# Performance work log

Hardware: AMD Instinct MI355X
Metric: run time of the kernel (lower is better)

The kernel has to match this reference:

```python
import jax, jax.numpy as jnp
import numpy as np

N_NODES = 50000
N_EDGES = 800000
NODE_DIM = 64
EDGE_DIM = 16
HIDDEN = 128
EPS = 1e-5


def _linear_init(key, fan_in, fan_out):
    k1, k2 = jax.random.split(key)
    bound = 1.0 / np.sqrt(fan_in)
    W = jax.random.uniform(k1, (fan_in, fan_out), minval=-bound, maxval=bound, dtype=jnp.float32)
    b = jax.random.uniform(k2, (fan_out,), minval=-bound, maxval=bound, dtype=jnp.float32)
    return W, b


def batchnorm(h, gamma, beta):
    # BatchNorm1d in training mode: batch mean/var (biased), eps=1e-5
    mu = jnp.mean(h, axis=0, keepdims=True)
    var = jnp.mean((h - mu) ** 2, axis=0, keepdims=True)
    return (h - mu) * jax.lax.rsqrt(var + EPS) * gamma + beta


def setup_inputs() -> dict:
    key = jax.random.key(0)
    ks = jax.random.split(key, 8)
    x = jax.random.normal(ks[0], (N_NODES, NODE_DIM), dtype=jnp.float32)
    edge_index = jax.random.randint(ks[1], (2, N_EDGES), 0, N_NODES, dtype=jnp.int64)
    edge_attr = jax.random.normal(ks[2], (N_EDGES, EDGE_DIM), dtype=jnp.float32)
    We1, be1 = _linear_init(ks[3], 2 * NODE_DIM + EDGE_DIM, HIDDEN)
    We2, be2 = _linear_init(ks[4], HIDDEN, HIDDEN)
    Wm, bm = _linear_init(ks[5], HIDDEN, HIDDEN)
    Wn1, bn1 = _linear_init(ks[6], NODE_DIM + HIDDEN, HIDDEN)
    Wn2, bn2 = _linear_init(ks[7], HIDDEN, HIDDEN)
    ones = jnp.ones((HIDDEN,), jnp.float32)
    zeros = jnp.zeros((HIDDEN,), jnp.float32)
    return dict(x=x, edge_index=edge_index, edge_attr=edge_attr,
                We1=We1, be1=be1, ge=ones, bbe=zeros, We2=We2, be2=be2,
                Wm=Wm, bm=bm,
                Wn1=Wn1, bn1=bn1, gn=ones, bbn=zeros, Wn2=Wn2, bn2=bn2)


def reference(x, edge_index, edge_attr, We1, be1, ge, bbe, We2, be2, Wm, bm, Wn1, bn1, gn, bbn, Wn2, bn2):
    row, col = edge_index[0], edge_index[1]
    # gather + concat -> edge network (Linear, BN, ReLU, Linear)
    edge_input = jnp.concatenate([x[row], x[col], edge_attr], axis=-1)  # [E, 2n+e]
    h = jax.nn.relu(batchnorm(edge_input @ We1 + be1, ge, bbe))
    edge_features = h @ We2 + be2
    # message MLP (Linear, ReLU)
    messages = jax.nn.relu(edge_features @ Wm + bm)  # [E, H]
    # scatter-add into source nodes
    agg = jax.ops.segment_sum(messages, row, num_segments=N_NODES)  # [N, H]
    # node network (Linear, BN, ReLU, Linear)
    node_input = jnp.concatenate([x, agg], axis=-1)
    hn = jax.nn.relu(batchnorm(node_input @ Wn1 + bn1, gn, bbn))
    return hn @ Wn2 + bn2
```

## Files before the change

kernel.cpp:

```cpp
#include <hip/hip_runtime.h>
#include <stdint.h>

#define NNODES 50000
#define NEDGES 800000
#define H 128
#define BN_EPS 1e-5f

typedef short short8 __attribute__((ext_vector_type(8)));
typedef short short4v __attribute__((ext_vector_type(4)));
typedef float f32x4 __attribute__((ext_vector_type(4)));

__device__ __forceinline__ float bf2f(unsigned short u) {
    unsigned int v = ((unsigned int)u) << 16;
    return __uint_as_float(v);
}
__device__ __forceinline__ unsigned short f2bf(float f) {
    unsigned int x = __float_as_uint(f);
    return (unsigned short)((x + 0x7FFFu + ((x >> 16) & 1u)) >> 16);
}
__device__ __forceinline__ short8 s8z() { short8 z = {0,0,0,0,0,0,0,0}; return z; }

template<int KB>
__device__ __forceinline__ void gemm_tile(const short* __restrict__ sA, const int SK,
                                          const unsigned short* __restrict__ WT, const int RK,
                                          const int n0, f32x4 acc[4][4], const int lane) {
    const int mr = lane & 15, quad = lane >> 4;
    const short* W = (const short*)WT;
    #pragma unroll
    for (int kb = 0; kb < KB; ++kb) {
        short8 a[4];
        #pragma unroll
        for (int mt = 0; mt < 4; ++mt)
            a[mt] = *(const short8*)&sA[(mt*16 + mr)*SK + kb*32 + quad*8];
        #pragma unroll
        for (int nt = 0; nt < 4; ++nt) {
            short8 b = *(const short8*)&W[(size_t)(n0 + nt*16 + mr)*RK + kb*32 + quad*8];
            #pragma unroll
            for (int mt = 0; mt < 4; ++mt)
                acc[mt][nt] = __builtin_amdgcn_mfma_f32_16x16x32_bf16(a[mt], b, acc[mt][nt], 0, 0, 0);
        }
    }
}

__global__ void k_fold(const float* __restrict__ We2, const float* __restrict__ be2,
                       const float* __restrict__ Wm, const float* __restrict__ bm,
                       float* __restrict__ W2m, float* __restrict__ b2m) {
    int j = threadIdx.x;
    int i = blockIdx.x;
    if (i < H) {
        float acc = 0.f;
        for (int k = 0; k < H; ++k) acc = fmaf(We2[i*H + k], Wm[k*H + j], acc);
        W2m[i*H + j] = acc;
    } else {
        float acc = bm[j];
        for (int k = 0; k < H; ++k) acc = fmaf(be2[k], Wm[k*H + j], acc);
        b2m[j] = acc;
    }
}

__global__ void k_prep2(const float* __restrict__ We1, const float* __restrict__ Wn1,
                        const float* __restrict__ Wn2,
                        unsigned short* __restrict__ WabT, unsigned short* __restrict__ Wn1T,
                        unsigned short* __restrict__ Wn2T, unsigned short* __restrict__ WcT,
                        int* __restrict__ cnt, float* __restrict__ S1f) {
    int i = blockIdx.x*256 + threadIdx.x;
    if (i < 16384) {
        int n = i >> 6, k = i & 63;
        WabT[n*64 + k] = f2bf(We1[(n < 128 ? k : 64 + k)*H + (n & 127)]);
    } else if (i < 40960) {
        int j = i - 16384; int n = j / 192, k = j - n*192;
        Wn1T[n*192 + k] = f2bf(Wn1[k*H + n]);
    } else if (i < 57344) {
        int j = i - 40960; int n = j >> 7, k = j & 127;
        Wn2T[n*H + k] = f2bf(Wn2[k*H + n]);
    } else if (i < 61440) {
        int j = i - 57344; int n = j >> 5, k = j & 31;
        WcT[n*32 + k] = (k < 16) ? f2bf(We1[(128 + k)*H + n]) : (unsigned short)0;
    } else if (i < 111440) {
        cnt[i - 61440] = 0;
    } else if (i < 112464) {
        S1f[i - 111440] = 0.f;
    }
}

__global__ void k_count(const int* __restrict__ ei, int* __restrict__ cnt) {
    int e = blockIdx.x*256 + threadIdx.x;
    if (e < NEDGES) atomicAdd(&cnt[ei[e]], 1);
}

__global__ void k_scanA(const int* __restrict__ cnt, int* __restrict__ bsum) {
    __shared__ int ws[4];
    const int tid = threadIdx.x;
    int i = blockIdx.x*256 + tid;
    int v = (i < NNODES) ? cnt[i] : 0;
    #pragma unroll
    for (int off = 32; off > 0; off >>= 1) v += __shfl_down(v, off);
    if ((tid & 63) == 0) ws[tid >> 6] = v;
    __syncthreads();
    if (tid == 0) bsum[blockIdx.x] = ws[0] + ws[1] + ws[2] + ws[3];
}

__global__ void k_scanB(const int* __restrict__ bsum, int* __restrict__ bpre,
                        int* __restrict__ offsets) {
    __shared__ int ws[4];
    const int tid = threadIdx.x;
    const int lane = tid & 63, wid = tid >> 6;
    int v = (tid < 196) ? bsum[tid] : 0;
    int xv = v;
    #pragma unroll
    for (int off = 1; off < 64; off <<= 1) {
        int y = __shfl_up(xv, off);
        if (lane >= off) xv += y;
    }
    if (lane == 63) ws[wid] = xv;
    __syncthreads();
    int base = 0;
    for (int w = 0; w < 4; ++w) if (w < wid) base += ws[w];
    int incl = base + xv;
    if (tid < 196) bpre[tid] = incl - v;
    if (tid == 255) offsets[NNODES] = incl;
}

__global__ void k_scanC(const int* __restrict__ cnt, const int* __restrict__ bpre,
                        int* __restrict__ offsets, int* __restrict__ cursor) {
    __shared__ int ws[4];
    const int tid = threadIdx.x;
    const int lane = tid & 63, wid = tid >> 6;
    int i = blockIdx.x*256 + tid;
    int v = (i < NNODES) ? cnt[i] : 0;
    int xv = v;
    #pragma unroll
    for (int off = 1; off < 64; off <<= 1) {
        int y = __shfl_up(xv, off);
        if (lane >= off) xv += y;
    }
    if (lane == 63) ws[wid] = xv;
    __syncthreads();
    int base = bpre[blockIdx.x];
    for (int w = 0; w < 4; ++w) if (w < wid) base += ws[w];
    int excl = base + xv - v;
    if (i < NNODES) { offsets[i] = excl; cursor[i] = excl; }
}

__global__ void k_scatter(const int* __restrict__ ei, int* __restrict__ cursor,
                          int* __restrict__ elist) {
    int e = blockIdx.x*256 + threadIdx.x;
    if (e < NEDGES) {
        int p = atomicAdd(&cursor[ei[e]], 1);
        elist[p] = e;
    }
}

__launch_bounds__(256)
__global__ void k_T(const float* __restrict__ x, const unsigned short* __restrict__ WabT,
                    unsigned short* __restrict__ T) {
    __shared__ short sA[128*72];
    const int tid = threadIdx.x;
    const int n0b = blockIdx.x*128;
    {
        const int rowl = tid >> 1, half = (tid & 1)*32;
        const int node = n0b + rowl;
        const bool ok = node < NNODES;
        #pragma unroll
        for (int c = 0; c < 4; ++c) {
            int k0 = half + c*8;
            short8 o = s8z();
            if (ok) {
                float4 a = *(const float4*)&x[node*64 + k0];
                float4 b = *(const float4*)&x[node*64 + k0 + 4];
                o[0]=(short)f2bf(a.x); o[1]=(short)f2bf(a.y); o[2]=(short)f2bf(a.z); o[3]=(short)f2bf(a.w);
                o[4]=(short)f2bf(b.x); o[5]=(short)f2bf(b.y); o[6]=(short)f2bf(b.z); o[7]=(short)f2bf(b.w);
            }
            *(short8*)&sA[rowl*72 + k0] = o;
        }
    }
    __syncthreads();
    const int wave = tid >> 6, lane = tid & 63;
    const int m0 = (wave & 1)*64;
    const int n0 = blockIdx.y*128 + (wave >> 1)*64;
    f32x4 acc[4][4];
    f32x4 z = {0.f, 0.f, 0.f, 0.f};
    #pragma unroll
    for (int mt = 0; mt < 4; ++mt)
        #pragma unroll
        for (int nt = 0; nt < 4; ++nt) acc[mt][nt] = z;
    gemm_tile<2>(sA + m0*72, 72, WabT, 64, n0, acc, lane);
    const int mr = lane & 15, quad = lane >> 4;
    #pragma unroll
    for (int nt = 0; nt < 4; ++nt) {
        int j = n0 + nt*16 + mr;
        #pragma unroll
        for (int mt = 0; mt < 4; ++mt) {
            int nb = n0b + m0 + mt*16 + quad*4;
            #pragma unroll
            for (int r = 0; r < 4; ++r) {
                int node = nb + r;
                if (node < NNODES) T[(size_t)node*256 + j] = f2bf(acc[mt][nt][r]);
            }
        }
    }
}

__launch_bounds__(256, 4)
__global__ void k_pass1(const unsigned short* __restrict__ T, const int* __restrict__ ei,
                        const int* __restrict__ elist, const float* __restrict__ ea,
                        const unsigned short* __restrict__ WcT, const float* __restrict__ be1,
                        unsigned short* __restrict__ eaP,
                        float* __restrict__ gS, float* __restrict__ gSS) {
    __shared__ short sT[128*136];
    __shared__ float sS[H], sSS[H];
    const int tid = threadIdx.x;
    const int p0 = blockIdx.x*128;
    const int wave = tid >> 6, lane = tid & 63;
    const int mr = lane & 15, quad = lane >> 4;
    const int mbase = wave*32;
    if (tid < 128) { sS[tid] = 0.f; sSS[tid] = 0.f; }
    const int lp = tid >> 1, half = tid & 1;
    const int e = elist[p0 + lp];
    const bool eaActive = (quad < 2);
    int e0i = 0, e1i = 0;
    if (eaActive) {
        e0i = elist[p0 + mbase + mr];
        e1i = elist[p0 + mbase + 16 + mr];
    }
    const int row = ei[e], col = ei[NEDGES + e];
    f32x4 u0, u1, v0, v1;
    if (eaActive) {
        u0 = __builtin_nontemporal_load((const f32x4*)&ea[(size_t)e0i*16 + quad*8]);
        u1 = __builtin_nontemporal_load((const f32x4*)&ea[(size_t)e0i*16 + quad*8 + 4]);
        v0 = __builtin_nontemporal_load((const f32x4*)&ea[(size_t)e1i*16 + quad*8]);
        v1 = __builtin_nontemporal_load((const f32x4*)&ea[(size_t)e1i*16 + quad*8 + 4]);
    }
    const unsigned short* Tr = &T[(size_t)row*256 + half*64];
    const unsigned short* Tc = &T[(size_t)col*256 + 128 + half*64];
    short8 t1[8], t2[8];
    #pragma unroll
    for (int c = 0; c < 8; ++c) t1[c] = *(const short8*)&Tr[c*8];
    #pragma unroll
    for (int c = 0; c < 8; ++c) t2[c] = *(const short8*)&Tc[c*8];
    __builtin_amdgcn_sched_barrier(0);
    short8 a0 = s8z(), a1 = s8z();
    if (eaActive) {
        a0[0]=(short)f2bf(u0[0]); a0[1]=(short)f2bf(u0[1]); a0[2]=(short)f2bf(u0[2]); a0[3]=(short)f2bf(u0[3]);
        a0[4]=(short)f2bf(u1[0]); a0[5]=(short)f2bf(u1[1]); a0[6]=(short)f2bf(u1[2]); a0[7]=(short)f2bf(u1[3]);
        a1[0]=(short)f2bf(v0[0]); a1[1]=(short)f2bf(v0[1]); a1[2]=(short)f2bf(v0[2]); a1[3]=(short)f2bf(v0[3]);
        a1[4]=(short)f2bf(v1[0]); a1[5]=(short)f2bf(v1[1]); a1[6]=(short)f2bf(v1[2]); a1[7]=(short)f2bf(v1[3]);
        *(short8*)&eaP[(size_t)(p0 + mbase + mr)*16 + quad*8] = a0;
        *(short8*)&eaP[(size_t)(p0 + mbase + 16 + mr)*16 + quad*8] = a1;
    }
    #pragma unroll
    for (int c = 0; c < 8; ++c) {
        short8 o;
        #pragma unroll
        for (int i = 0; i < 8; ++i)
            o[i] = (short)f2bf(bf2f((unsigned short)t1[c][i]) + bf2f((unsigned short)t2[c][i]));
        *(short8*)&sT[lp*136 + half*64 + c*8] = o;
    }
    f32x4 acc[2][8];
    f32x4 z = {0.f, 0.f, 0.f, 0.f};
    #pragma unroll
    for (int mt = 0; mt < 2; ++mt)
        #pragma unroll
        for (int nt = 0; nt < 8; ++nt) acc[mt][nt] = z;
    #pragma unroll
    for (int nt = 0; nt < 8; ++nt) {
        short8 b = *(const short8*)&WcT[(nt*16 + mr)*32 + quad*8];
        acc[0][nt] = __builtin_amdgcn_mfma_f32_16x16x32_bf16(a0, b, acc[0][nt], 0, 0, 0);
        acc[1][nt] = __builtin_amdgcn_mfma_f32_16x16x32_bf16(a1, b, acc[1][nt], 0, 0, 0);
    }
    __syncthreads();
    #pragma unroll
    for (int nt = 0; nt < 8; ++nt) {
        int j = nt*16 + mr;
        float bia = be1[j];
        float s = 0.f, ssum = 0.f;
        #pragma unroll
        for (int mt = 0; mt < 2; ++mt) {
            #pragma unroll
            for (int r = 0; r < 4; ++r) {
                int m = mbase + mt*16 + quad*4 + r;
                float v = acc[mt][nt][r] + bf2f((unsigned short)sT[m*136 + j]) + bia;
                s += v; ssum += v*v;
            }
        }
        s += __shfl_xor(s, 16);
        ssum += __shfl_xor(ssum, 16);
        s += __shfl_xor(s, 32);
        ssum += __shfl_xor(ssum, 32);
        if (quad == 0) {
            atomicAdd(&sS[j], s);
            atomicAdd(&sSS[j], ssum);
        }
    }
    __syncthreads();
    if (tid < 128) { atomicAdd(&gS[tid], sS[tid]); atomicAdd(&gSS[tid], sSS[tid]); }
}

__global__ void k_stats(const float* __restrict__ S, const float* __restrict__ SS,
                        const float* __restrict__ g, const float* __restrict__ b,
                        float invCount, float* __restrict__ scale, float* __restrict__ shift) {
    int j = threadIdx.x;
    float mu = S[j]*invCount;
    float var = SS[j]*invCount - mu*mu;
    float sc = rsqrtf(var + BN_EPS)*g[j];
    scale[j] = sc;
    shift[j] = b[j] - mu*sc;
}

__global__ void k_prep3(const float* __restrict__ W2m, const float* __restrict__ scale,
                        const float* __restrict__ shift, unsigned short* __restrict__ W2mST,
                        float* __restrict__ tvec, float* __restrict__ agg) {
    int i = blockIdx.x*256 + threadIdx.x;
    if (i < 16384) {
        int n = i >> 7, k = i & 127;
        W2mST[n*H + k] = f2bf(scale[k] * W2m[k*H + n]);
    } else if (i < 16512) {
        int k = i - 16384;
        tvec[k] = shift[k] / scale[k];
    } else if (i < 16512 + NNODES*H) {
        agg[i - 16512] = 0.f;
    }
}

__launch_bounds__(256, 4)
__global__ void k_pass2(const unsigned short* __restrict__ T, const int* __restrict__ ei,
                        const int* __restrict__ elist, const unsigned short* __restrict__ eaP,
                        const unsigned short* __restrict__ WcT, const float* __restrict__ be1,
                        const float* __restrict__ tvec, const unsigned short* __restrict__ W2mST,
                        const float* __restrict__ b2m, const int* __restrict__ offsets,
                        float* __restrict__ agg) {
    __shared__ short sT[128*136];
    __shared__ int rows[128];
    __shared__ int segStart[130];
    __shared__ int wcnt[2];
    __shared__ int nsegS;
    const int tid = threadIdx.x;
    const int p0 = blockIdx.x*128;
    const int wave = tid >> 6, lane = tid & 63;
    const int mr = lane & 15, quad = lane >> 4;
    const int mbase = wave*32;
    const int lp = tid >> 1, half = tid & 1;
    const int e = elist[p0 + lp];
    const int row = ei[e], col = ei[NEDGES + e];
    if (half == 0) rows[lp] = row;
    short8 a0 = s8z(), a1 = s8z();
    if (quad < 2) {
        a0 = *(const short8*)&eaP[(size_t)(p0 + mbase + mr)*16 + quad*8];
        a1 = *(const short8*)&eaP[(size_t)(p0 + mbase + 16 + mr)*16 + quad*8];
    }
    const unsigned short* Tr = &T[(size_t)row*256 + half*64];
    const unsigned short* Tc = &T[(size_t)col*256 + 128 + half*64];
    short8 t1[8], t2[8];
    #pragma unroll
    for (int c = 0; c < 8; ++c) t1[c] = *(const short8*)&Tr[c*8];
    #pragma unroll
    for (int c = 0; c < 8; ++c) t2[c] = *(const short8*)&Tc[c*8];
    __builtin_amdgcn_sched_barrier(0);
    #pragma unroll
    for (int c = 0; c < 8; ++c) {
        short8 o;
        #pragma unroll
        for (int i = 0; i < 8; ++i)
            o[i] = (short)f2bf(bf2f((unsigned short)t1[c][i]) + bf2f((unsigned short)t2[c][i]));
        *(short8*)&sT[lp*136 + half*64 + c*8] = o;
    }
    f32x4 accE[2][8];
    f32x4 z = {0.f, 0.f, 0.f, 0.f};
    #pragma unroll
    for (int mt = 0; mt < 2; ++mt)
        #pragma unroll
        for (int nt = 0; nt < 8; ++nt) accE[mt][nt] = z;
    #pragma unroll
    for (int nt = 0; nt < 8; ++nt) {
        short8 b = *(const short8*)&WcT[(nt*16 + mr)*32 + quad*8];
        accE[0][nt] = __builtin_amdgcn_mfma_f32_16x16x32_bf16(a0, b, accE[0][nt], 0, 0, 0);
        accE[1][nt] = __builtin_amdgcn_mfma_f32_16x16x32_bf16(a1, b, accE[1][nt], 0, 0, 0);
    }
    __syncthreads();
    int pre = 0, st = 0;
    if (tid < 128) {
        int r0 = rows[tid];
        st = (tid == 0) || (rows[tid - 1] != r0);
        unsigned long long m = __ballot(st);
        int lane2 = tid & 63;
        pre = __popcll(m & ((1ull << lane2) - 1ull));
        if (lane2 == 63) wcnt[tid >> 6] = pre + st;
    }
    __syncthreads();
    if (tid < 128) {
        int base = (tid >= 64) ? wcnt[0] : 0;
        int sid = base + pre + st - 1;
        if (st) segStart[sid] = tid;
        if (tid == 127) {
            int ns = wcnt[0] + wcnt[1];
            nsegS = ns;
            segStart[ns] = 128;
        }
    }
    #pragma unroll
    for (int nt = 0; nt < 8; ++nt) {
        int j = nt*16 + mr;
        float bia = be1[j];
        #pragma unroll
        for (int mt = 0; mt < 2; ++mt) {
            #pragma unroll
            for (int r = 0; r < 4; ++r) {
                int m = mbase + mt*16 + quad*4 + r;
                float v = accE[mt][nt][r] + bf2f((unsigned short)sT[m*136 + j]) + bia;
                sT[m*136 + j] = (short)f2bf(v);
            }
        }
    }
    short8 raw[4][2];
    #pragma unroll
    for (int kb = 0; kb < 4; ++kb)
        #pragma unroll
        for (int mt = 0; mt < 2; ++mt)
            raw[kb][mt] = *(const short8*)&sT[(mbase + mt*16 + mr)*136 + kb*32 + quad*8];
    f32x4 acc[2][8];
    #pragma unroll
    for (int mt = 0; mt < 2; ++mt)
        #pragma unroll
        for (int nt = 0; nt < 8; ++nt) acc[mt][nt] = z;
    #pragma unroll
    for (int kb = 0; kb < 4; ++kb) {
        float4 tq0 = *(const float4*)&tvec[kb*32 + quad*8];
        float4 tq1 = *(const float4*)&tvec[kb*32 + quad*8 + 4];
        short8 a[2];
        #pragma unroll
        for (int mt = 0; mt < 2; ++mt) {
            short8 rw = raw[kb][mt];
            short8 av;
            av[0] = (short)f2bf(fmaxf(bf2f((unsigned short)rw[0]) + tq0.x, 0.f));
            av[1] = (short)f2bf(fmaxf(bf2f((unsigned short)rw[1]) + tq0.y, 0.f));
            av[2] = (short)f2bf(fmaxf(bf2f((unsigned short)rw[2]) + tq0.z, 0.f));
            av[3] = (short)f2bf(fmaxf(bf2f((unsigned short)rw[3]) + tq0.w, 0.f));
            av[4] = (short)f2bf(fmaxf(bf2f((unsigned short)rw[4]) + tq1.x, 0.f));
            av[5] = (short)f2bf(fmaxf(bf2f((unsigned short)rw[5]) + tq1.y, 0.f));
            av[6] = (short)f2bf(fmaxf(bf2f((unsigned short)rw[6]) + tq1.z, 0.f));
            av[7] = (short)f2bf(fmaxf(bf2f((unsigned short)rw[7]) + tq1.w, 0.f));
            a[mt] = av;
        }
        #pragma unroll
        for (int nt = 0; nt < 8; ++nt) {
            short8 b = *(const short8*)&W2mST[(nt*16 + mr)*H + kb*32 + quad*8];
            acc[0][nt] = __builtin_amdgcn_mfma_f32_16x16x32_bf16(a[0], b, acc[0][nt], 0, 0, 0);
            acc[1][nt] = __builtin_amdgcn_mfma_f32_16x16x32_bf16(a[1], b, acc[1][nt], 0, 0, 0);
        }
    }
    #pragma unroll
    for (int nt = 0; nt < 8; ++nt) {
        int j = nt*16 + mr;
        float bias = b2m[j];
        #pragma unroll
        for (int mt = 0; mt < 2; ++mt) {
            #pragma unroll
            for (int r = 0; r < 4; ++r) {
                int m = mbase + mt*16 + quad*4 + r;
                sT[m*136 + j] = (short)f2bf(fmaxf(acc[mt][nt][r] + bias, 0.f));
            }
        }
    }
    __syncthreads();
    const int nseg = nsegS;
    for (int idx = tid; idx < (nseg << 5); idx += 256) {
        int s = idx >> 5, g = idx & 31;
        int j0 = g*4;
        int a0s = segStart[s], b0s = segStart[s + 1];
        float s0 = 0.f, s1 = 0.f, s2 = 0.f, s3 = 0.f;
        for (int i = a0s; i < b0s; ++i) {
            short4v v = *(const short4v*)&sT[i*136 + j0];
            s0 += bf2f((unsigned short)v[0]);
            s1 += bf2f((unsigned short)v[1]);
            s2 += bf2f((unsigned short)v[2]);
            s3 += bf2f((unsigned short)v[3]);
        }
        int r = rows[a0s];
        bool interior = (a0s > 0) && (b0s < 128);
        bool full = interior || ((p0 + a0s == offsets[r]) && (p0 + b0s == offsets[r + 1]));
        float* dst = &agg[(size_t)r*H + j0];
        if (full) {
            f32x4 o = {s0, s1, s2, s3};
            *(f32x4*)dst = o;
        } else {
            atomicAdd(dst + 0, s0);
            atomicAdd(dst + 1, s1);
            atomicAdd(dst + 2, s2);
            atomicAdd(dst + 3, s3);
        }
    }
}

__launch_bounds__(256)
__global__ void k_node1(const float* __restrict__ x, const float* __restrict__ agg,
                        const unsigned short* __restrict__ Wn1T, const float* __restrict__ bn1,
                        float* __restrict__ h2, float* __restrict__ gS, float* __restrict__ gSS) {
    __shared__ short sA[128*200];
    __shared__ float sS[H], sSS[H];
    const int tid = threadIdx.x;
    if (tid < H) { sS[tid] = 0.f; sSS[tid] = 0.f; }
    const int n0b = blockIdx.x*128;
    {
        const int rowl = tid >> 1, half = (tid & 1)*96;
        const int node = n0b + rowl;
        const bool ok = node < NNODES;
        #pragma unroll
        for (int c = 0; c < 12; ++c) {
            int k0 = half + c*8;
            short8 o = s8z();
            if (ok) {
                float4 a, b;
                if (k0 < 64) {
                    a = *(const float4*)&x[node*64 + k0];
                    b = *(const float4*)&x[node*64 + k0 + 4];
                } else {
                    a = *(const float4*)&agg[(size_t)node*H + (k0 - 64)];
                    b = *(const float4*)&agg[(size_t)node*H + (k0 - 64) + 4];
                }
                o[0]=(short)f2bf(a.x); o[1]=(short)f2bf(a.y); o[2]=(short)f2bf(a.z); o[3]=(short)f2bf(a.w);
                o[4]=(short)f2bf(b.x); o[5]=(short)f2bf(b.y); o[6]=(short)f2bf(b.z); o[7]=(short)f2bf(b.w);
            }
            *(short8*)&sA[rowl*200 + k0] = o;
        }
    }
    __syncthreads();
    const int wave = tid >> 6, lane = tid & 63;
    const int m0 = (wave & 1)*64, n0 = (wave >> 1)*64;
    f32x4 acc[4][4];
    f32x4 z = {0.f, 0.f, 0.f, 0.f};
    #pragma unroll
    for (int mt = 0; mt < 4; ++mt)
        #pragma unroll
        for (int nt = 0; nt < 4; ++nt) acc[mt][nt] = z;
    gemm_tile<6>(sA + m0*200, 200, Wn1T, 192, n0, acc, lane);
    const int mr = lane & 15, quad = lane >> 4;
    #pragma unroll
    for (int nt = 0; nt < 4; ++nt) {
        int j = n0 + nt*16 + mr;
        float bias = bn1[j];
        float s = 0.f, ssum = 0.f;
        #pragma unroll
        for (int mt = 0; mt < 4; ++mt) {
            int nb = n0b + m0 + mt*16 + quad*4;
            #pragma unroll
            for (int r = 0; r < 4; ++r) {
                int node = nb + r;
                if (node < NNODES) {
                    float v = acc[mt][nt][r] + bias;
                    h2[(size_t)node*H + j] = v;
                    s += v; ssum += v*v;
                }
            }
        }
        atomicAdd(&sS[j], s);
        atomicAdd(&sSS[j], ssum);
    }
    __syncthreads();
    if (tid < H) { atomicAdd(&gS[tid], sS[tid]); atomicAdd(&gSS[tid], sSS[tid]); }
}

__launch_bounds__(256)
__global__ void k_node2(const float* __restrict__ h2, const float* __restrict__ scale,
                        const float* __restrict__ shift, const unsigned short* __restrict__ Wn2T,
                        const float* __restrict__ bn2, float* __restrict__ out) {
    __shared__ short sA[128*136];
    const int tid = threadIdx.x;
    const int n0b = blockIdx.x*128;
    {
        const int rowl = tid >> 1, half = (tid & 1)*64;
        const int node = n0b + rowl;
        const bool ok = node < NNODES;
        #pragma unroll
        for (int c = 0; c < 8; ++c) {
            int k0 = half + c*8;
            short8 o = s8z();
            if (ok) {
                float4 a = *(const float4*)&h2[(size_t)node*H + k0];
                float4 b = *(const float4*)&h2[(size_t)node*H + k0 + 4];
                float4 sc0 = *(const float4*)&scale[k0], sc1 = *(const float4*)&scale[k0 + 4];
                float4 sh0 = *(const float4*)&shift[k0], sh1 = *(const float4*)&shift[k0 + 4];
                o[0] = (short)f2bf(fmaxf(fmaf(a.x, sc0.x, sh0.x), 0.f));
                o[1] = (short)f2bf(fmaxf(fmaf(a.y, sc0.y, sh0.y), 0.f));
                o[2] = (short)f2bf(fmaxf(fmaf(a.z, sc0.z, sh0.z), 0.f));
                o[3] = (short)f2bf(fmaxf(fmaf(a.w, sc0.w, sh0.w), 0.f));
                o[4] = (short)f2bf(fmaxf(fmaf(b.x, sc1.x, sh1.x), 0.f));
                o[5] = (short)f2bf(fmaxf(fmaf(b.y, sc1.y, sh1.y), 0.f));
                o[6] = (short)f2bf(fmaxf(fmaf(b.z, sc1.z, sh1.z), 0.f));
                o[7] = (short)f2bf(fmaxf(fmaf(b.w, sc1.w, sh1.w), 0.f));
            }
            *(short8*)&sA[rowl*136 + k0] = o;
        }
    }
    __syncthreads();
    const int wave = tid >> 6, lane = tid & 63;
    const int m0 = (wave & 1)*64, n0 = (wave >> 1)*64;
    f32x4 acc[4][4];
    f32x4 z = {0.f, 0.f, 0.f, 0.f};
    #pragma unroll
    for (int mt = 0; mt < 4; ++mt)
        #pragma unroll
        for (int nt = 0; nt < 4; ++nt) acc[mt][nt] = z;
    gemm_tile<4>(sA + m0*136, 136, Wn2T, 128, n0, acc, lane);
    const int mr = lane & 15, quad = lane >> 4;
    #pragma unroll
    for (int nt = 0; nt < 4; ++nt) {
        int j = n0 + nt*16 + mr;
        float bias = bn2[j];
        #pragma unroll
        for (int mt = 0; mt < 4; ++mt) {
            int nb = n0b + m0 + mt*16 + quad*4;
            #pragma unroll
            for (int r = 0; r < 4; ++r) {
                int node = nb + r;
                if (node < NNODES) out[(size_t)node*H + j] = acc[mt][nt][r] + bias;
            }
        }
    }
}

extern "C" void kernel_launch(void* const* d_in, const int* in_sizes, int n_in,
                              void* d_out, int out_size, void* d_ws, size_t ws_size,
                              hipStream_t stream) {
    (void)in_sizes; (void)n_in; (void)out_size; (void)ws_size;
    const float* x   = (const float*)d_in[0];
    const int*   ei  = (const int*)d_in[1];
    const float* ea  = (const float*)d_in[2];
    const float* We1 = (const float*)d_in[3];
    const float* be1 = (const float*)d_in[4];
    const float* ge  = (const float*)d_in[5];
    const float* bbe = (const float*)d_in[6];
    const float* We2 = (const float*)d_in[7];
    const float* be2 = (const float*)d_in[8];
    const float* Wm  = (const float*)d_in[9];
    const float* bm  = (const float*)d_in[10];
    const float* Wn1 = (const float*)d_in[11];
    const float* bn1 = (const float*)d_in[12];
    const float* gn  = (const float*)d_in[13];
    const float* bbn = (const float*)d_in[14];
    const float* Wn2 = (const float*)d_in[15];
    const float* bn2 = (const float*)d_in[16];
    float* out = (float*)d_out;

    char* ws = (char*)d_ws;
    unsigned short* eaP  = (unsigned short*)(ws);
    float*          h2   = (float*)(ws);
    float*          agg  = (float*)(ws + 204800000);
    unsigned short* Tbuf = (unsigned short*)(ws + 230400000);
    int* cnt     = (int*)(ws + 256000000);
    int* offsets = (int*)(ws + 256200192);
    int* cursor  = (int*)(ws + 256400448);
    int* bsum    = (int*)(ws + 256600448);
    int* bpre    = (int*)(ws + 256601472);
    int* elist   = (int*)(ws + 256602496);
    float* S1     = (float*)(ws + 259802496);
    float* SS1    = S1 + 128;
    float* S2     = S1 + 256;
    float* SS2    = S1 + 384;
    float* scale1 = S1 + 512;
    float* shift1 = S1 + 640;
    float* scale2 = S1 + 768;
    float* shift2 = S1 + 896;
    float* W2m  = (float*)(ws + 259806592);
    float* b2m  = (float*)(ws + 259872128);
    float* tvec = (float*)(ws + 259872640);
    unsigned short* WabT  = (unsigned short*)(ws + 259873152);
    unsigned short* Wn1T  = (unsigned short*)(ws + 259905920);
    unsigned short* Wn2T  = (unsigned short*)(ws + 259955072);
    unsigned short* W2mST = (unsigned short*)(ws + 259987840);
    unsigned short* WcT   = (unsigned short*)(ws + 260020608);

    k_fold<<<H + 1, H, 0, stream>>>(We2, be2, Wm, bm, W2m, b2m);
    k_prep2<<<440, 256, 0, stream>>>(We1, Wn1, Wn2, WabT, Wn1T, Wn2T, WcT, cnt, S1);
    k_count<<<NEDGES/256, 256, 0, stream>>>(ei, cnt);
    k_scanA<<<196, 256, 0, stream>>>(cnt, bsum);
    k_scanB<<<1, 256, 0, stream>>>(bsum, bpre, offsets);
    k_scanC<<<196, 256, 0, stream>>>(cnt, bpre, offsets, cursor);
    k_scatter<<<NEDGES/256, 256, 0, stream>>>(ei, cursor, elist);
    k_T<<<dim3(391, 2), 256, 0, stream>>>(x, WabT, Tbuf);
    k_pass1<<<NEDGES/128, 256, 0, stream>>>(Tbuf, ei, elist, ea, WcT, be1, eaP, S1, SS1);
    k_stats<<<1, H, 0, stream>>>(S1, SS1, ge, bbe, 1.0f/NEDGES, scale1, shift1);
    k_prep3<<<12565, 256, 0, stream>>>(W2m, scale1, shift1, W2mST, tvec, agg);
    k_pass2<<<NEDGES/128, 256, 0, stream>>>(Tbuf, ei, elist, eaP, WcT, be1, tvec, W2mST,
                                            b2m, offsets, agg);
    k_node1<<<391, 256, 0, stream>>>(x, agg, Wn1T, bn1, h2, S2, SS2);
    k_stats<<<1, H, 0, stream>>>(S2, SS2, gn, bbn, 1.0f/NNODES, scale2, shift2);
    k_node2<<<391, 256, 0, stream>>>(h2, scale2, shift2, Wn2T, bn2, out);
}
```

Before: 658.3 us.

## Replace per-node projection table with per-edge MFMA on gathered bf16 features

New measurement: 766.1 us. 16.4% more time.

```diff
diff --git a/kernel.cpp b/kernel.cpp
--- a/kernel.cpp
+++ b/kernel.cpp
@@ -60,13 +60,13 @@
 
 __global__ void k_prep2(const float* __restrict__ We1, const float* __restrict__ Wn1,
                         const float* __restrict__ Wn2,
-                        unsigned short* __restrict__ WabT, unsigned short* __restrict__ Wn1T,
+                        unsigned short* __restrict__ Wab2T, unsigned short* __restrict__ Wn1T,
                         unsigned short* __restrict__ Wn2T, unsigned short* __restrict__ WcT,
                         int* __restrict__ cnt, float* __restrict__ S1f) {
     int i = blockIdx.x*256 + threadIdx.x;
     if (i < 16384) {
-        int n = i >> 6, k = i & 63;
-        WabT[n*64 + k] = f2bf(We1[(n < 128 ? k : 64 + k)*H + (n & 127)]);
+        int n = i >> 7, k = i & 127;
+        Wab2T[n*128 + k] = f2bf(We1[k*H + n]);
     } else if (i < 40960) {
         int j = i - 16384; int n = j / 192, k = j - n*192;
         Wn1T[n*192 + k] = f2bf(Wn1[k*H + n]);
@@ -83,6 +83,18 @@
     }
 }
 
+__global__ void k_xb(const float* __restrict__ x, unsigned short* __restrict__ xb) {
+    int i = blockIdx.x*256 + threadIdx.x;
+    if (i < NNODES*8) {
+        float4 a = *(const float4*)&x[i*8];
+        float4 b = *(const float4*)&x[i*8 + 4];
+        short8 o;
+        o[0]=(short)f2bf(a.x); o[1]=(short)f2bf(a.y); o[2]=(short)f2bf(a.z); o[3]=(short)f2bf(a.w);
+        o[4]=(short)f2bf(b.x); o[5]=(short)f2bf(b.y); o[6]=(short)f2bf(b.z); o[7]=(short)f2bf(b.w);
+        *(short8*)&xb[i*8] = o;
+    }
+}
+
 __global__ void k_count(const int* __restrict__ ei, int* __restrict__ cnt) {
     int e = blockIdx.x*256 + threadIdx.x;
     if (e < NEDGES) atomicAdd(&cnt[ei[e]], 1);
@@ -151,63 +163,14 @@
     }
 }
 
-__launch_bounds__(256)
-__global__ void k_T(const float* __restrict__ x, const unsigned short* __restrict__ WabT,
-                    unsigned short* __restrict__ T) {
-    __shared__ short sA[128*72];
-    const int tid = threadIdx.x;
-    const int n0b = blockIdx.x*128;
-    {
-        const int rowl = tid >> 1, half = (tid & 1)*32;
-        const int node = n0b + rowl;
-        const bool ok = node < NNODES;
-        #pragma unroll
-        for (int c = 0; c < 4; ++c) {
-            int k0 = half + c*8;
-            short8 o = s8z();
-            if (ok) {
-                float4 a = *(const float4*)&x[node*64 + k0];
-                float4 b = *(const float4*)&x[node*64 + k0 + 4];
-                o[0]=(short)f2bf(a.x); o[1]=(short)f2bf(a.y); o[2]=(short)f2bf(a.z); o[3]=(short)f2bf(a.w);
-                o[4]=(short)f2bf(b.x); o[5]=(short)f2bf(b.y); o[6]=(short)f2bf(b.z); o[7]=(short)f2bf(b.w);
-            }
-            *(short8*)&sA[rowl*72 + k0] = o;
-        }
-    }
-    __syncthreads();
-    const int wave = tid >> 6, lane = tid & 63;
-    const int m0 = (wave & 1)*64;
-    const int n0 = blockIdx.y*128 + (wave >> 1)*64;
-    f32x4 acc[4][4];
-    f32x4 z = {0.f, 0.f, 0.f, 0.f};
-    #pragma unroll
-    for (int mt = 0; mt < 4; ++mt)
-        #pragma unroll
-        for (int nt = 0; nt < 4; ++nt) acc[mt][nt] = z;
-    gemm_tile<2>(sA + m0*72, 72, WabT, 64, n0, acc, lane);
-    const int mr = lane & 15, quad = lane >> 4;
-    #pragma unroll
-    for (int nt = 0; nt < 4; ++nt) {
-        int j = n0 + nt*16 + mr;
-        #pragma unroll
-        for (int mt = 0; mt < 4; ++mt) {
-            int nb = n0b + m0 + mt*16 + quad*4;
-            #pragma unroll
-            for (int r = 0; r < 4; ++r) {
-                int node = nb + r;
-                if (node < NNODES) T[(size_t)node*256 + j] = f2bf(acc[mt][nt][r]);
-            }
-        }
-    }
-}
-
 __launch_bounds__(256, 4)
-__global__ void k_pass1(const unsigned short* __restrict__ T, const int* __restrict__ ei,
+__global__ void k_pass1(const unsigned short* __restrict__ xb, const int* __restrict__ ei,
                         const int* __restrict__ elist, const float* __restrict__ ea,
+                        const unsigned short* __restrict__ Wab2T,
                         const unsigned short* __restrict__ WcT, const float* __restrict__ be1,
                         unsigned short* __restrict__ eaP,
                         float* __restrict__ gS, float* __restrict__ gSS) {
-    __shared__ short sT[128*136];
+    __shared__ short sA[128*136];
     __shared__ float sS[H], sSS[H];
     const int tid = threadIdx.x;
     const int p0 = blockIdx.x*128;
@@ -223,7 +186,7 @@
         e0i = elist[p0 + mbase + mr];
         e1i = elist[p0 + mbase + 16 + mr];
     }
-    const int row = ei[e], col = ei[NEDGES + e];
+    const int node = ei[half*NEDGES + e];
     f32x4 u0, u1, v0, v1;
     if (eaActive) {
         u0 = __builtin_nontemporal_load((const f32x4*)&ea[(size_t)e0i*16 + quad*8]);
@@ -231,13 +194,10 @@
         v0 = __builtin_nontemporal_load((const f32x4*)&ea[(size_t)e1i*16 + quad*8]);
         v1 = __builtin_nontemporal_load((const f32x4*)&ea[(size_t)e1i*16 + quad*8 + 4]);
     }
-    const unsigned short* Tr = &T[(size_t)row*256 + half*64];
-    const unsigned short* Tc = &T[(size_t)col*256 + 128 + half*64];
-    short8 t1[8], t2[8];
-    #pragma unroll
-    for (int c = 0; c < 8; ++c) t1[c] = *(const short8*)&Tr[c*8];
-    #pragma unroll
-    for (int c = 0; c < 8; ++c) t2[c] = *(const short8*)&Tc[c*8];
+    const unsigned short* Xs = &xb[(size_t)node*64];
+    short8 t[8];
+    #pragma unroll
+    for (int c = 0; c < 8; ++c) t[c] = *(const short8*)&Xs[c*8];
     __builtin_amdgcn_sched_barrier(0);
     short8 a0 = s8z(), a1 = s8z();
     if (eaActive) {
@@ -249,13 +209,8 @@
         *(short8*)&eaP[(size_t)(p0 + mbase + 16 + mr)*16 + quad*8] = a1;
     }
     #pragma unroll
-    for (int c = 0; c < 8; ++c) {
-        short8 o;
-        #pragma unroll
-        for (int i = 0; i < 8; ++i)
-            o[i] = (short)f2bf(bf2f((unsigned short)t1[c][i]) + bf2f((unsigned short)t2[c][i]));
-        *(short8*)&sT[lp*136 + half*64 + c*8] = o;
-    }
+    for (int c = 0; c < 8; ++c)
+        *(short8*)&sA[lp*136 + half*64 + c*8] = t[c];
     f32x4 acc[2][8];
     f32x4 z = {0.f, 0.f, 0.f, 0.f};
     #pragma unroll
@@ -270,6 +225,19 @@
     }
     __syncthreads();
     #pragma unroll
+    for (int kb = 0; kb < 4; ++kb) {
+        short8 a[2];
+        #pragma unroll
+        for (int mt = 0; mt < 2; ++mt)
+            a[mt] = *(const short8*)&sA[(mbase + mt*16 + mr)*136 + kb*32 + quad*8];
+        #pragma unroll
+        for (int nt = 0; nt < 8; ++nt) {
+            short8 b = *(const short8*)&Wab2T[(nt*16 + mr)*128 + kb*32 + quad*8];
+            acc[0][nt] = __builtin_amdgcn_mfma_f32_16x16x32_bf16(a[0], b, acc[0][nt], 0, 0, 0);
+            acc[1][nt] = __builtin_amdgcn_mfma_f32_16x16x32_bf16(a[1], b, acc[1][nt], 0, 0, 0);
+        }
+    }
+    #pragma unroll
     for (int nt = 0; nt < 8; ++nt) {
         int j = nt*16 + mr;
         float bia = be1[j];
@@ -278,8 +246,7 @@
         for (int mt = 0; mt < 2; ++mt) {
             #pragma unroll
             for (int r = 0; r < 4; ++r) {
-                int m = mbase + mt*16 + quad*4 + r;
-                float v = acc[mt][nt][r] + bf2f((unsigned short)sT[m*136 + j]) + bia;
+                float v = acc[mt][nt][r] + bia;
                 s += v; ssum += v*v;
             }
         }
@@ -323,8 +290,9 @@
 }
 
 __launch_bounds__(256, 4)
-__global__ void k_pass2(const unsigned short* __restrict__ T, const int* __restrict__ ei,
+__global__ void k_pass2(const unsigned short* __restrict__ xb, const int* __restrict__ ei,
                         const int* __restrict__ elist, const unsigned short* __restrict__ eaP,
+                        const unsigned short* __restrict__ Wab2T,
                         const unsigned short* __restrict__ WcT, const float* __restrict__ be1,
                         const float* __restrict__ tvec, const unsigned short* __restrict__ W2mST,
                         const float* __restrict__ b2m, const int* __restrict__ offsets,
@@ -341,29 +309,21 @@
     const int mbase = wave*32;
     const int lp = tid >> 1, half = tid & 1;
     const int e = elist[p0 + lp];
-    const int row = ei[e], col = ei[NEDGES + e];
-    if (half == 0) rows[lp] = row;
+    const int node = ei[half*NEDGES + e];
+    if (half == 0) rows[lp] = node;
     short8 a0 = s8z(), a1 = s8z();
     if (quad < 2) {
         a0 = *(const short8*)&eaP[(size_t)(p0 + mbase + mr)*16 + quad*8];
         a1 = *(const short8*)&eaP[(size_t)(p0 + mbase + 16 + mr)*16 + quad*8];
     }
-    const unsigned short* Tr = &T[(size_t)row*256 + half*64];
-    const unsigned short* Tc = &T[(size_t)col*256 + 128 + half*64];
-    short8 t1[8], t2[8];
-    #pragma unroll
-    for (int c = 0; c < 8; ++c) t1[c] = *(const short8*)&Tr[c*8];
-    #pragma unroll
-    for (int c = 0; c < 8; ++c) t2[c] = *(const short8*)&Tc[c*8];
+    const unsigned short* Xs = &xb[(size_t)node*64];
+    short8 t[8];
+    #pragma unroll
+    for (int c = 0; c < 8; ++c) t[c] = *(const short8*)&Xs[c*8];
     __builtin_amdgcn_sched_barrier(0);
     #pragma unroll
-    for (int c = 0; c < 8; ++c) {
-        short8 o;
-        #pragma unroll
-        for (int i = 0; i < 8; ++i)
-            o[i] = (short)f2bf(bf2f((unsigned short)t1[c][i]) + bf2f((unsigned short)t2[c][i]));
-        *(short8*)&sT[lp*136 + half*64 + c*8] = o;
-    }
+    for (int c = 0; c < 8; ++c)
+        *(short8*)&sT[lp*136 + half*64 + c*8] = t[c];
     f32x4 accE[2][8];
     f32x4 z = {0.f, 0.f, 0.f, 0.f};
     #pragma unroll
@@ -386,6 +346,19 @@
         pre = __popcll(m & ((1ull << lane2) - 1ull));
         if (lane2 == 63) wcnt[tid >> 6] = pre + st;
     }
+    #pragma unroll
+    for (int kb = 0; kb < 4; ++kb) {
+        short8 a[2];
+        #pragma unroll
+        for (int mt = 0; mt < 2; ++mt)
+            a[mt] = *(const short8*)&sT[(mbase + mt*16 + mr)*136 + kb*32 + quad*8];
+        #pragma unroll
+        for (int nt = 0; nt < 8; ++nt) {
+            short8 b = *(const short8*)&Wab2T[(nt*16 + mr)*128 + kb*32 + quad*8];
+            accE[0][nt] = __builtin_amdgcn_mfma_f32_16x16x32_bf16(a[0], b, accE[0][nt], 0, 0, 0);
+            accE[1][nt] = __builtin_amdgcn_mfma_f32_16x16x32_bf16(a[1], b, accE[1][nt], 0, 0, 0);
+        }
+    }
     __syncthreads();
     if (tid < 128) {
         int base = (tid >= 64) ? wcnt[0] : 0;
@@ -406,8 +379,7 @@
             #pragma unroll
             for (int r = 0; r < 4; ++r) {
                 int m = mbase + mt*16 + quad*4 + r;
-                float v = accE[mt][nt][r] + bf2f((unsigned short)sT[m*136 + j]) + bia;
-                sT[m*136 + j] = (short)f2bf(v);
+                sT[m*136 + j] = (short)f2bf(accE[mt][nt][r] + bia);
             }
         }
     }
@@ -645,7 +617,7 @@
     unsigned short* eaP  = (unsigned short*)(ws);
     float*          h2   = (float*)(ws);
     float*          agg  = (float*)(ws + 204800000);
-    unsigned short* Tbuf = (unsigned short*)(ws + 230400000);
+    unsigned short* xb   = (unsigned short*)(ws + 230400000);
     int* cnt     = (int*)(ws + 256000000);
     int* offsets = (int*)(ws + 256200192);
     int* cursor  = (int*)(ws + 256400448);
@@ -663,24 +635,24 @@
     float* W2m  = (float*)(ws + 259806592);
     float* b2m  = (float*)(ws + 259872128);
     float* tvec = (float*)(ws + 259872640);
-    unsigned short* WabT  = (unsigned short*)(ws + 259873152);
+    unsigned short* Wab2T = (unsigned short*)(ws + 259873152);
     unsigned short* Wn1T  = (unsigned short*)(ws + 259905920);
     unsigned short* Wn2T  = (unsigned short*)(ws + 259955072);
     unsigned short* W2mST = (unsigned short*)(ws + 259987840);
     unsigned short* WcT   = (unsigned short*)(ws + 260020608);
 
     k_fold<<<H + 1, H, 0, stream>>>(We2, be2, Wm, bm, W2m, b2m);
-    k_prep2<<<440, 256, 0, stream>>>(We1, Wn1, Wn2, WabT, Wn1T, Wn2T, WcT, cnt, S1);
+    k_prep2<<<440, 256, 0, stream>>>(We1, Wn1, Wn2, Wab2T, Wn1T, Wn2T, WcT, cnt, S1);
+    k_xb<<<1563, 256, 0, stream>>>(x, xb);
     k_count<<<NEDGES/256, 256, 0, stream>>>(ei, cnt);
     k_scanA<<<196, 256, 0, stream>>>(cnt, bsum);
     k_scanB<<<1, 256, 0, stream>>>(bsum, bpre, offsets);
     k_scanC<<<196, 256, 0, stream>>>(cnt, bpre, offsets, cursor);
     k_scatter<<<NEDGES/256, 256, 0, stream>>>(ei, cursor, elist);
-    k_T<<<dim3(391, 2), 256, 0, stream>>>(x, WabT, Tbuf);
-    k_pass1<<<NEDGES/128, 256, 0, stream>>>(Tbuf, ei, elist, ea, WcT, be1, eaP, S1, SS1);
+    k_pass1<<<NEDGES/128, 256, 0, stream>>>(xb, ei, elist, ea, Wab2T, WcT, be1, eaP, S1, SS1);
     k_stats<<<1, H, 0, stream>>>(S1, SS1, ge, bbe, 1.0f/NEDGES, scale1, shift1);
     k_prep3<<<12565, 256, 0, stream>>>(W2m, scale1, shift1, W2mST, tvec, agg);
-    k_pass2<<<NEDGES/128, 256, 0, stream>>>(Tbuf, ei, elist, eaP, WcT, be1, tvec, W2mST,
+    k_pass2<<<NEDGES/128, 256, 0, stream>>>(xb, ei, elist, eaP, Wab2T, WcT, be1, tvec, W2mST,
                                             b2m, offsets, agg);
     k_node1<<<391, 256, 0, stream>>>(x, agg, Wn1T, bn1, h2, S2, SS2);
     k_stats<<<1, H, 0, stream>>>(S2, SS2, gn, bbn, 1.0f/NNODES, scale2, shift2);
```
